# Kernel optimization log

Hardware: AMD Instinct MI355X
Metric: run time of the kernel (lower is better)

The kernel has to match this reference:

```python
import jax, jax.numpy as jnp
import numpy as np

INPUT_SIZE = 512
HIDDEN_SIZE = 512


def setup_inputs() -> dict:
    key = jax.random.key(0)
    k1, k2, k3, k4, k5 = jax.random.split(key, 5)
    B, N = 8, 2048
    x = jax.random.normal(k1, (B, N, INPUT_SIZE), dtype=jnp.float32)
    # Linear params (torch nn.Linear: y = x @ W^T + b), init scale ~ 1/sqrt(fan_in)
    s = 1.0 / np.sqrt(INPUT_SIZE)
    Wq = jax.random.uniform(k2, (HIDDEN_SIZE, INPUT_SIZE), minval=-s, maxval=s, dtype=jnp.float32)
    bq = jax.random.uniform(k3, (HIDDEN_SIZE,), minval=-s, maxval=s, dtype=jnp.float32)
    Wk = jax.random.uniform(k4, (HIDDEN_SIZE, INPUT_SIZE), minval=-s, maxval=s, dtype=jnp.float32)
    bk = jax.random.uniform(k5, (HIDDEN_SIZE,), minval=-s, maxval=s, dtype=jnp.float32)
    return {"x": x, "Wq": Wq, "bq": bq, "Wk": Wk, "bk": bk}


def reference(x, Wq, bq, Wk, bk):
    # q, k: [B, N, H]
    q = jnp.einsum('bnd,hd->bnh', x, Wq) + bq
    k = jnp.einsum('bnd,hd->bnh', x, Wk) + bk
    # scores: [B, N, N], softmax over last axis (dim=2)
    scores = jnp.einsum('bnh,bmh->bnm', q, k) / jnp.sqrt(jnp.float32(HIDDEN_SIZE))
    attn = jax.nn.softmax(scores, axis=2)
    # attended = attn^T @ x : [B, N, input_size]; squeeze(2) no-op since input_size>1
    attended = jnp.einsum('bnm,bnd->bmd', attn, x)
    return attended
```

## Files before the change

kernel.cpp:

```cpp
#include <hip/hip_runtime.h>

typedef __bf16 bf16x8 __attribute__((ext_vector_type(8)));
typedef float f32x4 __attribute__((ext_vector_type(4)));

__device__ __forceinline__ ushort f2bf(float f) {
    union { float f; unsigned u; } v; v.f = f;
    unsigned r = v.u + 0x7FFF + ((v.u >> 16) & 1);
    return (ushort)(r >> 16);
}

__device__ __forceinline__ void async_copy16(const void* g, void* l) {
    __builtin_amdgcn_global_load_lds(
        (const __attribute__((address_space(1))) void*)g,
        (__attribute__((address_space(3))) void*)l, 16, 0, 0);
}

__global__ __launch_bounds__(256) void cvt_kernel(
    const float4* __restrict__ x, const float4* __restrict__ Wq,
    const float4* __restrict__ Wk, const float4* __restrict__ bq,
    const float4* __restrict__ bk,
    ushort4* __restrict__ xb, ushort4* __restrict__ Wb,
    float4* __restrict__ biasc) {
    int i = blockIdx.x * 256 + threadIdx.x;
    if (i < 2097152) {
        float4 v = x[i];
        ushort4 r; r.x = f2bf(v.x); r.y = f2bf(v.y); r.z = f2bf(v.z); r.w = f2bf(v.w);
        xb[i] = r;
    }
    if (i < 131072) {
        float4 v = (i < 65536) ? Wq[i] : Wk[i - 65536];
        ushort4 r; r.x = f2bf(v.x); r.y = f2bf(v.y); r.z = f2bf(v.z); r.w = f2bf(v.w);
        Wb[i] = r;
    }
    if (i < 256) {
        biasc[i] = (i < 128) ? bq[i] : bk[i - 128];
    }
}

__global__ __launch_bounds__(256) void fold_kernel(
    const float* __restrict__ x, const float* __restrict__ Z,
    ushort* __restrict__ xzT) {
    __shared__ float tile[64][65];
    __shared__ float zin[64];
    const int b = blockIdx.y;
    const int td = blockIdx.x & 7;
    const int tn = blockIdx.x >> 3;
    const int n0 = tn * 64, d0 = td * 64;
    const int t = threadIdx.x;
    if (t < 64) zin[t] = 1.0f / Z[b * 2048 + n0 + t];
    __syncthreads();
    const int c = t & 63, r0 = t >> 6;
#pragma unroll
    for (int j = 0; j < 16; ++j) {
        int r = r0 + j * 4;
        tile[r][c] = x[((size_t)b * 2048 + n0 + r) * 512 + d0 + c] * zin[r];
    }
    __syncthreads();
#pragma unroll
    for (int j = 0; j < 16; ++j) {
        int dr = r0 + j * 4;
        xzT[((size_t)b * 512 + d0 + dr) * 2048 + n0 + c] = f2bf(tile[c][dr]);
    }
}

template <int EPI>
__global__ __launch_bounds__(256) void gemm_bt(
    const ushort* __restrict__ A, int lda, long sA,
    const ushort* __restrict__ B, int ldb, long sB,
    void* __restrict__ C, int ldc, long sC,
    int M, int N, int K,
    const float* __restrict__ bias, float scale,
    float* __restrict__ Z, long sZ) {
    __shared__ ushort lA[128 * 64];
    __shared__ ushort lB[128 * 64];
    const int b = blockIdx.y;
    A += (size_t)b * sA;
    B += (size_t)b * sB;
    const int tiles_n = N >> 7;
    const int tm = blockIdx.x / tiles_n, tn = blockIdx.x % tiles_n;
    const int t = threadIdx.x;
    const int l = t & 63, w = t >> 6;
    const int wr = w >> 1, wc = w & 1;

    f32x4 acc[4][4];
#pragma unroll
    for (int i = 0; i < 4; ++i)
#pragma unroll
        for (int j = 0; j < 4; ++j) acc[i][j] = (f32x4){0.f, 0.f, 0.f, 0.f};

    for (int k0 = 0; k0 < K; k0 += 64) {
#pragma unroll
        for (int p = 0; p < 4; ++p) {
            int off = p * 4096 + t * 16;
            int row = off >> 7;
            int kb = off & 127;
            int kswz = kb ^ ((row & 7) << 4);
            const ushort* srcA = A + (size_t)(tm * 128 + row) * lda + k0 + (kswz >> 1);
            async_copy16(srcA, (char*)lA + off);
            const ushort* srcB = B + (size_t)(tn * 128 + row) * ldb + k0 + (kswz >> 1);
            async_copy16(srcB, (char*)lB + off);
        }
        __syncthreads();
#pragma unroll
        for (int ks = 0; ks < 2; ++ks) {
            bf16x8 af[4], bfr[4];
#pragma unroll
            for (int i = 0; i < 4; ++i) {
                int row = wr * 64 + i * 16 + (l & 15);
                int colb = (ks * 64 + (l >> 4) * 16) ^ ((row & 7) << 4);
                af[i] = *(const bf16x8*)((const char*)lA + row * 128 + colb);
            }
#pragma unroll
            for (int j = 0; j < 4; ++j) {
                int row = wc * 64 + j * 16 + (l & 15);
                int colb = (ks * 64 + (l >> 4) * 16) ^ ((row & 7) << 4);
                bfr[j] = *(const bf16x8*)((const char*)lB + row * 128 + colb);
            }
#pragma unroll
            for (int i = 0; i < 4; ++i)
#pragma unroll
                for (int j = 0; j < 4; ++j)
                    acc[i][j] = __builtin_amdgcn_mfma_f32_16x16x32_bf16(
                        af[i], bfr[j], acc[i][j], 0, 0, 0);
        }
        __syncthreads();
    }

    const int m_base = tm * 128 + wr * 64;
    const int n_base = tn * 128 + wc * 64;

    if (EPI == 0) {
        ushort* Cp = (ushort*)C + (size_t)b * sC;
#pragma unroll
        for (int i = 0; i < 4; ++i)
#pragma unroll
            for (int j = 0; j < 4; ++j)
#pragma unroll
                for (int q = 0; q < 4; ++q) {
                    int row = m_base + i * 16 + (l >> 4) * 4 + q;
                    int col = n_base + j * 16 + (l & 15);
                    Cp[(size_t)row * ldc + col] = f2bf(acc[i][j][q] + bias[col]);
                }
    } else if (EPI == 1) {
        ushort* Cp = (ushort*)C + (size_t)b * sC;
        float colsum[4] = {0.f, 0.f, 0.f, 0.f};
#pragma unroll
        for (int i = 0; i < 4; ++i)
#pragma unroll
            for (int j = 0; j < 4; ++j)
#pragma unroll
                for (int q = 0; q < 4; ++q) {
                    int row = m_base + i * 16 + (l >> 4) * 4 + q;
                    int col = n_base + j * 16 + (l & 15);
                    float e = __expf(acc[i][j][q] * scale);
                    Cp[(size_t)row * ldc + col] = f2bf(e);
                    colsum[j] += e;
                }
#pragma unroll
        for (int j = 0; j < 4; ++j) {
            float s = colsum[j];
            s += __shfl_xor(s, 16);
            s += __shfl_xor(s, 32);
            if (l < 16) atomicAdd(&Z[b * sZ + n_base + j * 16 + l], s);
        }
    } else {
        float* Cp = (float*)C + (size_t)b * sC;
#pragma unroll
        for (int i = 0; i < 4; ++i)
#pragma unroll
            for (int j = 0; j < 4; ++j)
#pragma unroll
                for (int q = 0; q < 4; ++q) {
                    int row = m_base + i * 16 + (l >> 4) * 4 + q;
                    int col = n_base + j * 16 + (l & 15);
                    Cp[(size_t)row * ldc + col] = acc[i][j][q];
                }
    }
}

extern "C" void kernel_launch(void* const* d_in, const int* in_sizes, int n_in,
                              void* d_out, int out_size, void* d_ws, size_t ws_size,
                              hipStream_t stream) {
    const float* x  = (const float*)d_in[0];
    const float* Wq = (const float*)d_in[1];
    const float* bq = (const float*)d_in[2];
    const float* Wk = (const float*)d_in[3];
    const float* bk = (const float*)d_in[4];

    char* ws = (char*)d_ws;
    ushort* xb    = (ushort*)(ws);
    ushort* Wb    = (ushort*)(ws + 16777216);
    float*  biasc = (float*) (ws + 17825792);
    float*  Z     = (float*) (ws + 17829888);
    ushort* qkb   = (ushort*)(ws + 17895424);
    ushort* E     = (ushort*)(ws + 51449856);
    ushort* xzT   = xb;

    hipMemsetAsync(Z, 0, 16384 * 4, stream);

    cvt_kernel<<<8192, 256, 0, stream>>>(
        (const float4*)x, (const float4*)Wq, (const float4*)Wk,
        (const float4*)bq, (const float4*)bk,
        (ushort4*)xb, (ushort4*)Wb, (float4*)biasc);

    gemm_bt<0><<<dim3(1024, 1), 256, 0, stream>>>(
        xb, 512, 0L, Wb, 512, 0L, qkb, 1024, 0L,
        16384, 1024, 512, biasc, 0.f, nullptr, 0L);

    gemm_bt<1><<<dim3(256, 8), 256, 0, stream>>>(
        qkb + 512, 1024, 2048L * 1024, qkb, 1024, 2048L * 1024,
        E, 2048, 2048L * 2048, 2048, 2048, 512,
        nullptr, 0.04419417382415922f, Z, 2048L);

    fold_kernel<<<dim3(256, 8), 256, 0, stream>>>(x, Z, xzT);

    gemm_bt<2><<<dim3(64, 8), 256, 0, stream>>>(
        E, 2048, 2048L * 2048, xzT, 2048, 512L * 2048,
        d_out, 512, 2048L * 512, 2048, 512, 2048,
        nullptr, 0.f, nullptr, 0L);
}
```

Before: 154.4 us.

## Rewrite GEMMs as 8-wave 256-row tiles with double-buffered async LDS pipeline

Replaces the 128x128 single-buffered GEMM with an 8-wave (512-thread) kernel using 256xBN tiles, dynamic shared memory, and double-buffered global-to-LDS async copies. The copies are interleaved with MFMA phases through explicit waitcnt, barriers and setprio, so loads overlap compute. A new swizzle layout is used for the K-halves. Larger tiles increase data reuse per block but reduce block count (e.g. 256 blocks for the projection, 256 for the last GEMM), which risks poor CU occupancy on a 256-CU device and adds heavy register pressure.

```diff
diff --git a/kernel.cpp b/kernel.cpp
--- a/kernel.cpp
+++ b/kernel.cpp
@@ -63,119 +63,189 @@
     }
 }
 
-template <int EPI>
-__global__ __launch_bounds__(256) void gemm_bt(
+template <int BN, int EPI>
+__global__ __launch_bounds__(512, 2) void gemm8(
     const ushort* __restrict__ A, int lda, long sA,
     const ushort* __restrict__ B, int ldb, long sB,
     void* __restrict__ C, int ldc, long sC,
-    int M, int N, int K,
+    int tiles_n, int K,
     const float* __restrict__ bias, float scale,
     float* __restrict__ Z, long sZ) {
-    __shared__ ushort lA[128 * 64];
-    __shared__ ushort lB[128 * 64];
+    constexpr int NREP = BN / 64;
+    constexpr int JW = NREP / 2;
+    constexpr int LB = BN / 128;
+    constexpr int VMN = 4 + 2 * LB;
+    constexpr int ABUF = 32768;
+    constexpr int BHALF = BN * 64;
+    constexpr int BBUF = 2 * BHALF;
+    extern __shared__ char smem[];
+    char* lA = smem;
+    char* lB = smem + 2 * ABUF;
+
     const int b = blockIdx.y;
-    A += (size_t)b * sA;
-    B += (size_t)b * sB;
-    const int tiles_n = N >> 7;
+    const ushort* Ag = A + (size_t)b * sA;
+    const ushort* Bg = B + (size_t)b * sB;
     const int tm = blockIdx.x / tiles_n, tn = blockIdx.x % tiles_n;
     const int t = threadIdx.x;
     const int l = t & 63, w = t >> 6;
-    const int wr = w >> 1, wc = w & 1;
-
-    f32x4 acc[4][4];
-#pragma unroll
-    for (int i = 0; i < 4; ++i)
-#pragma unroll
-        for (int j = 0; j < 4; ++j) acc[i][j] = (f32x4){0.f, 0.f, 0.f, 0.f};
-
-    for (int k0 = 0; k0 < K; k0 += 64) {
-#pragma unroll
-        for (int p = 0; p < 4; ++p) {
-            int off = p * 4096 + t * 16;
-            int row = off >> 7;
-            int kb = off & 127;
-            int kswz = kb ^ ((row & 7) << 4);
-            const ushort* srcA = A + (size_t)(tm * 128 + row) * lda + k0 + (kswz >> 1);
-            async_copy16(srcA, (char*)lA + off);
-            const ushort* srcB = B + (size_t)(tn * 128 + row) * ldb + k0 + (kswz >> 1);
-            async_copy16(srcB, (char*)lB + off);
+    const int wr = w >> 2, wc = w & 3;
+    const int NT = K >> 6;
+
+    size_t gA[2]; int dA[2];
+#pragma unroll
+    for (int p = 0; p < 2; ++p) {
+        int off = p * 8192 + t * 16;
+        int row = off >> 6, kb = off & 63;
+        int kbs = kb ^ ((row & 6) << 3);
+        gA[p] = (size_t)(tm * 256 + row) * lda + (kbs >> 1);
+        dA[p] = off;
+    }
+    size_t gB[LB]; int dB[LB];
+#pragma unroll
+    for (int p = 0; p < LB; ++p) {
+        int off = p * 8192 + t * 16;
+        int row = off >> 6, kb = off & 63;
+        int kbs = kb ^ ((row & 6) << 3);
+        gB[p] = (size_t)(tn * BN + row) * ldb + (kbs >> 1);
+        dB[p] = off;
+    }
+
+    auto stageA = [&](int db, int ks, int ktt) {
+        if (ktt > NT - 1) ktt = NT - 1;
+        const ushort* s0 = Ag + ktt * 64 + ks * 32;
+#pragma unroll
+        for (int p = 0; p < 2; ++p)
+            async_copy16(s0 + gA[p], lA + db * ABUF + ks * 16384 + dA[p]);
+    };
+    auto stageB = [&](int db, int ks, int ktt) {
+        if (ktt > NT - 1) ktt = NT - 1;
+        const ushort* s0 = Bg + ktt * 64 + ks * 32;
+#pragma unroll
+        for (int p = 0; p < LB; ++p)
+            async_copy16(s0 + gB[p], lB + db * BBUF + ks * BHALF + dB[p]);
+    };
+
+    const int lan = (l & 15) * 64 + ((((l >> 4)) ^ ((l >> 1) & 3)) << 4);
+
+    f32x4 acc[8][NREP];
+#pragma unroll
+    for (int i = 0; i < 8; ++i)
+#pragma unroll
+        for (int j = 0; j < NREP; ++j) acc[i][j] = (f32x4){0.f, 0.f, 0.f, 0.f};
+
+    stageA(0, 0, 0); stageB(0, 0, 0);
+    stageA(0, 1, 0); stageB(0, 1, 0);
+    stageA(1, 0, 1); stageB(1, 0, 1);
+    asm volatile("s_waitcnt vmcnt(%0)" :: "n"(VMN) : "memory");
+    __builtin_amdgcn_s_barrier();
+    __builtin_amdgcn_sched_barrier(0);
+
+    for (int kt = 0; kt < NT; ++kt) {
+        const int db = kt & 1;
+        bf16x8 a[8];
+#pragma unroll
+        for (int ph = 0; ph < 4; ++ph) {
+            const int ks = ph >> 1;
+            const int js = (ph == 1 || ph == 2) ? 1 : 0;
+            if (ph == 0 || ph == 2) {
+#pragma unroll
+                for (int i = 0; i < 8; ++i)
+                    a[i] = *(const bf16x8*)(lA + db * ABUF + ks * 16384 +
+                                            wr * 8192 + i * 1024 + lan);
+            }
+            bf16x8 bb[JW];
+#pragma unroll
+            for (int j = 0; j < JW; ++j)
+                bb[j] = *(const bf16x8*)(lB + db * BBUF + ks * BHALF +
+                                         wc * (BN / 4) * 64 + (js * JW + j) * 1024 + lan);
+            if (ph == 0)      stageA(db ^ 1, 1, kt + 1);
+            else if (ph == 1) stageB(db ^ 1, 1, kt + 1);
+            else if (ph == 2) stageA(db, 0, kt + 2);
+            else              stageB(db, 0, kt + 2);
+            __builtin_amdgcn_sched_barrier(0);
+            if (ph == 1 || ph == 3)
+                asm volatile("s_waitcnt vmcnt(%0)" :: "n"(VMN) : "memory");
+            __builtin_amdgcn_s_barrier();
+            __builtin_amdgcn_s_setprio(1);
+#pragma unroll
+            for (int i = 0; i < 8; ++i)
+#pragma unroll
+                for (int j = 0; j < JW; ++j)
+                    acc[i][js * JW + j] = __builtin_amdgcn_mfma_f32_16x16x32_bf16(
+                        a[i], bb[j], acc[i][js * JW + j], 0, 0, 0);
+            __builtin_amdgcn_s_setprio(0);
+            __builtin_amdgcn_s_barrier();
+            __builtin_amdgcn_sched_barrier(0);
         }
-        __syncthreads();
-#pragma unroll
-        for (int ks = 0; ks < 2; ++ks) {
-            bf16x8 af[4], bfr[4];
-#pragma unroll
-            for (int i = 0; i < 4; ++i) {
-                int row = wr * 64 + i * 16 + (l & 15);
-                int colb = (ks * 64 + (l >> 4) * 16) ^ ((row & 7) << 4);
-                af[i] = *(const bf16x8*)((const char*)lA + row * 128 + colb);
-            }
-#pragma unroll
-            for (int j = 0; j < 4; ++j) {
-                int row = wc * 64 + j * 16 + (l & 15);
-                int colb = (ks * 64 + (l >> 4) * 16) ^ ((row & 7) << 4);
-                bfr[j] = *(const bf16x8*)((const char*)lB + row * 128 + colb);
-            }
-#pragma unroll
-            for (int i = 0; i < 4; ++i)
-#pragma unroll
-                for (int j = 0; j < 4; ++j)
-                    acc[i][j] = __builtin_amdgcn_mfma_f32_16x16x32_bf16(
-                        af[i], bfr[j], acc[i][j], 0, 0, 0);
-        }
-        __syncthreads();
-    }
-
-    const int m_base = tm * 128 + wr * 64;
-    const int n_base = tn * 128 + wc * 64;
+    }
+    asm volatile("s_waitcnt vmcnt(0)" ::: "memory");
+
+    const int mb = tm * 256 + wr * 128;
+    const int nb = tn * BN + wc * (BN / 4);
 
     if (EPI == 0) {
         ushort* Cp = (ushort*)C + (size_t)b * sC;
 #pragma unroll
-        for (int i = 0; i < 4; ++i)
-#pragma unroll
-            for (int j = 0; j < 4; ++j)
+        for (int i = 0; i < 8; ++i)
+#pragma unroll
+            for (int j = 0; j < NREP; ++j)
 #pragma unroll
                 for (int q = 0; q < 4; ++q) {
-                    int row = m_base + i * 16 + (l >> 4) * 4 + q;
-                    int col = n_base + j * 16 + (l & 15);
+                    int row = mb + i * 16 + (l >> 4) * 4 + q;
+                    int col = nb + j * 16 + (l & 15);
                     Cp[(size_t)row * ldc + col] = f2bf(acc[i][j][q] + bias[col]);
                 }
     } else if (EPI == 1) {
         ushort* Cp = (ushort*)C + (size_t)b * sC;
-        float colsum[4] = {0.f, 0.f, 0.f, 0.f};
-#pragma unroll
-        for (int i = 0; i < 4; ++i)
-#pragma unroll
-            for (int j = 0; j < 4; ++j)
+        float colsum[NREP];
+#pragma unroll
+        for (int j = 0; j < NREP; ++j) colsum[j] = 0.f;
+#pragma unroll
+        for (int i = 0; i < 8; ++i)
+#pragma unroll
+            for (int j = 0; j < NREP; ++j)
 #pragma unroll
                 for (int q = 0; q < 4; ++q) {
-                    int row = m_base + i * 16 + (l >> 4) * 4 + q;
-                    int col = n_base + j * 16 + (l & 15);
+                    int row = mb + i * 16 + (l >> 4) * 4 + q;
+                    int col = nb + j * 16 + (l & 15);
                     float e = __expf(acc[i][j][q] * scale);
                     Cp[(size_t)row * ldc + col] = f2bf(e);
                     colsum[j] += e;
                 }
 #pragma unroll
-        for (int j = 0; j < 4; ++j) {
+        for (int j = 0; j < NREP; ++j) {
             float s = colsum[j];
             s += __shfl_xor(s, 16);
             s += __shfl_xor(s, 32);
-            if (l < 16) atomicAdd(&Z[b * sZ + n_base + j * 16 + l], s);
+            if (l < 16) atomicAdd(&Z[b * sZ + nb + j * 16 + l], s);
         }
     } else {
         float* Cp = (float*)C + (size_t)b * sC;
 #pragma unroll
-        for (int i = 0; i < 4; ++i)
-#pragma unroll
-            for (int j = 0; j < 4; ++j)
+        for (int i = 0; i < 8; ++i)
+#pragma unroll
+            for (int j = 0; j < NREP; ++j)
 #pragma unroll
                 for (int q = 0; q < 4; ++q) {
-                    int row = m_base + i * 16 + (l >> 4) * 4 + q;
-                    int col = n_base + j * 16 + (l & 15);
+                    int row = mb + i * 16 + (l >> 4) * 4 + q;
+                    int col = nb + j * 16 + (l & 15);
                     Cp[(size_t)row * ldc + col] = acc[i][j][q];
                 }
     }
+}
+
+namespace {
+struct AttrInit {
+    AttrInit() {
+        hipFuncSetAttribute(reinterpret_cast<const void*>(&gemm8<256, 0>),
+                            hipFuncAttributeMaxDynamicSharedMemorySize, 131072);
+        hipFuncSetAttribute(reinterpret_cast<const void*>(&gemm8<256, 1>),
+                            hipFuncAttributeMaxDynamicSharedMemorySize, 131072);
+        hipFuncSetAttribute(reinterpret_cast<const void*>(&gemm8<128, 2>),
+                            hipFuncAttributeMaxDynamicSharedMemorySize, 98304);
+    }
+};
+AttrInit attr_init_;
 }
 
 extern "C" void kernel_launch(void* const* d_in, const int* in_sizes, int n_in,
@@ -203,19 +273,19 @@
         (const float4*)bq, (const float4*)bk,
         (ushort4*)xb, (ushort4*)Wb, (float4*)biasc);
 
-    gemm_bt<0><<<dim3(1024, 1), 256, 0, stream>>>(
+    gemm8<256, 0><<<dim3(256, 1), 512, 131072, stream>>>(
         xb, 512, 0L, Wb, 512, 0L, qkb, 1024, 0L,
-        16384, 1024, 512, biasc, 0.f, nullptr, 0L);
-
-    gemm_bt<1><<<dim3(256, 8), 256, 0, stream>>>(
+        4, 512, biasc, 0.f, nullptr, 0L);
+
+    gemm8<256, 1><<<dim3(64, 8), 512, 131072, stream>>>(
         qkb + 512, 1024, 2048L * 1024, qkb, 1024, 2048L * 1024,
-        E, 2048, 2048L * 2048, 2048, 2048, 512,
+        E, 2048, 2048L * 2048, 8, 512,
         nullptr, 0.04419417382415922f, Z, 2048L);
 
     fold_kernel<<<dim3(256, 8), 256, 0, stream>>>(x, Z, xzT);
 
-    gemm_bt<2><<<dim3(64, 8), 256, 0, stream>>>(
+    gemm8<128, 2><<<dim3(32, 8), 512, 98304, stream>>>(
         E, 2048, 2048L * 2048, xzT, 2048, 512L * 2048,
-        d_out, 512, 2048L * 512, 2048, 512, 2048,
+        d_out, 512, 2048L * 512, 4, 2048,
         nullptr, 0.f, nullptr, 0L);
 }
```

Result: no change. 156.4 us (+1.3%).

## Switch GEMMs to 32x32x16 MFMA and read bf16 x in fold kernel

Applied to the files above, without the earlier changes.

Replaces the 16x16x32 bf16 MFMA tiles with 32x32x16 MFMA in all three GEMMs, with a matching epilogue layout. This reduces LDS fragment loads per MFMA and the instruction count. The fold kernel now reads the bf16 copy of x with vectorized ushort4 loads and stores, instead of fp32 x with scalar stores, which cuts its memory traffic. Its output is written into the qkb buffer, since xb is now read. Using bf16 x in the fold adds a second rounding step.

```diff
diff --git a/kernel.cpp b/kernel.cpp
--- a/kernel.cpp
+++ b/kernel.cpp
@@ -1,12 +1,16 @@
 #include <hip/hip_runtime.h>
 
 typedef __bf16 bf16x8 __attribute__((ext_vector_type(8)));
-typedef float f32x4 __attribute__((ext_vector_type(4)));
+typedef float f32x16 __attribute__((ext_vector_type(16)));
 
 __device__ __forceinline__ ushort f2bf(float f) {
     union { float f; unsigned u; } v; v.f = f;
     unsigned r = v.u + 0x7FFF + ((v.u >> 16) & 1);
     return (ushort)(r >> 16);
+}
+__device__ __forceinline__ float bf2f(ushort u) {
+    union { unsigned u; float f; } v; v.u = ((unsigned)u) << 16;
+    return v.f;
 }
 
 __device__ __forceinline__ void async_copy16(const void* g, void* l) {
@@ -38,7 +42,7 @@
 }
 
 __global__ __launch_bounds__(256) void fold_kernel(
-    const float* __restrict__ x, const float* __restrict__ Z,
+    const ushort* __restrict__ xb, const float* __restrict__ Z,
     ushort* __restrict__ xzT) {
     __shared__ float tile[64][65];
     __shared__ float zin[64];
@@ -49,26 +53,36 @@
     const int t = threadIdx.x;
     if (t < 64) zin[t] = 1.0f / Z[b * 2048 + n0 + t];
     __syncthreads();
-    const int c = t & 63, r0 = t >> 6;
-#pragma unroll
-    for (int j = 0; j < 16; ++j) {
-        int r = r0 + j * 4;
-        tile[r][c] = x[((size_t)b * 2048 + n0 + r) * 512 + d0 + c] * zin[r];
+    const int c4 = (t & 15) * 4, rr = t >> 4;
+#pragma unroll
+    for (int j = 0; j < 4; ++j) {
+        int nr = rr + j * 16;
+        ushort4 v = *(const ushort4*)&xb[((size_t)b * 2048 + n0 + nr) * 512 + d0 + c4];
+        float zi = zin[nr];
+        tile[nr][c4 + 0] = bf2f(v.x) * zi;
+        tile[nr][c4 + 1] = bf2f(v.y) * zi;
+        tile[nr][c4 + 2] = bf2f(v.z) * zi;
+        tile[nr][c4 + 3] = bf2f(v.w) * zi;
     }
     __syncthreads();
 #pragma unroll
-    for (int j = 0; j < 16; ++j) {
-        int dr = r0 + j * 4;
-        xzT[((size_t)b * 512 + d0 + dr) * 2048 + n0 + c] = f2bf(tile[c][dr]);
+    for (int j = 0; j < 4; ++j) {
+        int dr = rr + j * 16;
+        ushort4 r;
+        r.x = f2bf(tile[c4 + 0][dr]);
+        r.y = f2bf(tile[c4 + 1][dr]);
+        r.z = f2bf(tile[c4 + 2][dr]);
+        r.w = f2bf(tile[c4 + 3][dr]);
+        *(ushort4*)&xzT[((size_t)b * 512 + d0 + dr) * 2048 + n0 + c4] = r;
     }
 }
 
 template <int EPI>
-__global__ __launch_bounds__(256) void gemm_bt(
+__global__ __launch_bounds__(256) void gemm_bt32(
     const ushort* __restrict__ A, int lda, long sA,
     const ushort* __restrict__ B, int ldb, long sB,
     void* __restrict__ C, int ldc, long sC,
-    int M, int N, int K,
+    int tiles_n, int K,
     const float* __restrict__ bias, float scale,
     float* __restrict__ Z, long sZ) {
     __shared__ ushort lA[128 * 64];
@@ -76,105 +90,114 @@
     const int b = blockIdx.y;
     A += (size_t)b * sA;
     B += (size_t)b * sB;
-    const int tiles_n = N >> 7;
     const int tm = blockIdx.x / tiles_n, tn = blockIdx.x % tiles_n;
     const int t = threadIdx.x;
     const int l = t & 63, w = t >> 6;
     const int wr = w >> 1, wc = w & 1;
 
-    f32x4 acc[4][4];
-#pragma unroll
-    for (int i = 0; i < 4; ++i)
-#pragma unroll
-        for (int j = 0; j < 4; ++j) acc[i][j] = (f32x4){0.f, 0.f, 0.f, 0.f};
+    f32x16 acc[2][2];
+#pragma unroll
+    for (int i = 0; i < 2; ++i)
+#pragma unroll
+        for (int j = 0; j < 2; ++j)
+#pragma unroll
+            for (int q = 0; q < 16; ++q) acc[i][j][q] = 0.f;
+
+    const int soff = t * 16;
+    const int srow0 = soff >> 7;
+    const int skb = soff & 127;
 
     for (int k0 = 0; k0 < K; k0 += 64) {
 #pragma unroll
         for (int p = 0; p < 4; ++p) {
-            int off = p * 4096 + t * 16;
-            int row = off >> 7;
-            int kb = off & 127;
-            int kswz = kb ^ ((row & 7) << 4);
-            const ushort* srcA = A + (size_t)(tm * 128 + row) * lda + k0 + (kswz >> 1);
-            async_copy16(srcA, (char*)lA + off);
-            const ushort* srcB = B + (size_t)(tn * 128 + row) * ldb + k0 + (kswz >> 1);
-            async_copy16(srcB, (char*)lB + off);
+            int off = p * 4096 + soff;
+            int row = srow0 + p * 32;
+            int kswz = skb ^ ((row & 7) << 4);
+            async_copy16(A + (size_t)(tm * 128 + row) * lda + k0 + (kswz >> 1),
+                         (char*)lA + off);
+            async_copy16(B + (size_t)(tn * 128 + row) * ldb + k0 + (kswz >> 1),
+                         (char*)lB + off);
         }
         __syncthreads();
 #pragma unroll
-        for (int ks = 0; ks < 2; ++ks) {
-            bf16x8 af[4], bfr[4];
-#pragma unroll
-            for (int i = 0; i < 4; ++i) {
-                int row = wr * 64 + i * 16 + (l & 15);
-                int colb = (ks * 64 + (l >> 4) * 16) ^ ((row & 7) << 4);
-                af[i] = *(const bf16x8*)((const char*)lA + row * 128 + colb);
-            }
-#pragma unroll
-            for (int j = 0; j < 4; ++j) {
-                int row = wc * 64 + j * 16 + (l & 15);
-                int colb = (ks * 64 + (l >> 4) * 16) ^ ((row & 7) << 4);
-                bfr[j] = *(const bf16x8*)((const char*)lB + row * 128 + colb);
-            }
-#pragma unroll
-            for (int i = 0; i < 4; ++i)
-#pragma unroll
-                for (int j = 0; j < 4; ++j)
-                    acc[i][j] = __builtin_amdgcn_mfma_f32_16x16x32_bf16(
-                        af[i], bfr[j], acc[i][j], 0, 0, 0);
+        for (int ksx = 0; ksx < 4; ++ksx) {
+            bf16x8 af[2], bfr[2];
+#pragma unroll
+            for (int rb = 0; rb < 2; ++rb) {
+                int row = wr * 64 + rb * 32 + (l & 31);
+                int colb = (ksx * 32 + (l >> 5) * 16) ^ ((row & 7) << 4);
+                af[rb] = *(const bf16x8*)((const char*)lA + row * 128 + colb);
+            }
+#pragma unroll
+            for (int cb = 0; cb < 2; ++cb) {
+                int row = wc * 64 + cb * 32 + (l & 31);
+                int colb = (ksx * 32 + (l >> 5) * 16) ^ ((row & 7) << 4);
+                bfr[cb] = *(const bf16x8*)((const char*)lB + row * 128 + colb);
+            }
+#pragma unroll
+            for (int rb = 0; rb < 2; ++rb)
+#pragma unroll
+                for (int cb = 0; cb < 2; ++cb)
+                    acc[rb][cb] = __builtin_amdgcn_mfma_f32_32x32x16_bf16(
+                        af[rb], bfr[cb], acc[rb][cb], 0, 0, 0);
         }
         __syncthreads();
     }
 
-    const int m_base = tm * 128 + wr * 64;
-    const int n_base = tn * 128 + wc * 64;
+    const int mb = tm * 128 + wr * 64;
+    const int nb = tn * 128 + wc * 64;
+    const int rbase = 4 * (l >> 5);
+    const int cl = l & 31;
 
     if (EPI == 0) {
         ushort* Cp = (ushort*)C + (size_t)b * sC;
 #pragma unroll
-        for (int i = 0; i < 4; ++i)
-#pragma unroll
-            for (int j = 0; j < 4; ++j)
-#pragma unroll
-                for (int q = 0; q < 4; ++q) {
-                    int row = m_base + i * 16 + (l >> 4) * 4 + q;
-                    int col = n_base + j * 16 + (l & 15);
-                    Cp[(size_t)row * ldc + col] = f2bf(acc[i][j][q] + bias[col]);
+        for (int rb = 0; rb < 2; ++rb)
+#pragma unroll
+            for (int cb = 0; cb < 2; ++cb) {
+                int col = nb + cb * 32 + cl;
+                float bv = bias[col];
+#pragma unroll
+                for (int reg = 0; reg < 16; ++reg) {
+                    int row = mb + rb * 32 + (reg & 3) + 8 * (reg >> 2) + rbase;
+                    Cp[(size_t)row * ldc + col] = f2bf(acc[rb][cb][reg] + bv);
                 }
+            }
     } else if (EPI == 1) {
         ushort* Cp = (ushort*)C + (size_t)b * sC;
-        float colsum[4] = {0.f, 0.f, 0.f, 0.f};
-#pragma unroll
-        for (int i = 0; i < 4; ++i)
-#pragma unroll
-            for (int j = 0; j < 4; ++j)
-#pragma unroll
-                for (int q = 0; q < 4; ++q) {
-                    int row = m_base + i * 16 + (l >> 4) * 4 + q;
-                    int col = n_base + j * 16 + (l & 15);
-                    float e = __expf(acc[i][j][q] * scale);
+        float cs[2] = {0.f, 0.f};
+#pragma unroll
+        for (int rb = 0; rb < 2; ++rb)
+#pragma unroll
+            for (int cb = 0; cb < 2; ++cb) {
+                int col = nb + cb * 32 + cl;
+#pragma unroll
+                for (int reg = 0; reg < 16; ++reg) {
+                    int row = mb + rb * 32 + (reg & 3) + 8 * (reg >> 2) + rbase;
+                    float e = __expf(acc[rb][cb][reg] * scale);
                     Cp[(size_t)row * ldc + col] = f2bf(e);
-                    colsum[j] += e;
+                    cs[cb] += e;
                 }
-#pragma unroll
-        for (int j = 0; j < 4; ++j) {
-            float s = colsum[j];
-            s += __shfl_xor(s, 16);
+            }
+#pragma unroll
+        for (int cb = 0; cb < 2; ++cb) {
+            float s = cs[cb];
             s += __shfl_xor(s, 32);
-            if (l < 16) atomicAdd(&Z[b * sZ + n_base + j * 16 + l], s);
+            if (l < 32) atomicAdd(&Z[b * sZ + nb + cb * 32 + cl], s);
         }
     } else {
         float* Cp = (float*)C + (size_t)b * sC;
 #pragma unroll
-        for (int i = 0; i < 4; ++i)
-#pragma unroll
-            for (int j = 0; j < 4; ++j)
-#pragma unroll
-                for (int q = 0; q < 4; ++q) {
-                    int row = m_base + i * 16 + (l >> 4) * 4 + q;
-                    int col = n_base + j * 16 + (l & 15);
-                    Cp[(size_t)row * ldc + col] = acc[i][j][q];
+        for (int rb = 0; rb < 2; ++rb)
+#pragma unroll
+            for (int cb = 0; cb < 2; ++cb) {
+                int col = nb + cb * 32 + cl;
+#pragma unroll
+                for (int reg = 0; reg < 16; ++reg) {
+                    int row = mb + rb * 32 + (reg & 3) + 8 * (reg >> 2) + rbase;
+                    Cp[(size_t)row * ldc + col] = acc[rb][cb][reg];
                 }
+            }
     }
 }
 
@@ -194,7 +217,7 @@
     float*  Z     = (float*) (ws + 17829888);
     ushort* qkb   = (ushort*)(ws + 17895424);
     ushort* E     = (ushort*)(ws + 51449856);
-    ushort* xzT   = xb;
+    ushort* xzT   = qkb;
 
     hipMemsetAsync(Z, 0, 16384 * 4, stream);
 
@@ -203,19 +226,19 @@
         (const float4*)bq, (const float4*)bk,
         (ushort4*)xb, (ushort4*)Wb, (float4*)biasc);
 
-    gemm_bt<0><<<dim3(1024, 1), 256, 0, stream>>>(
+    gemm_bt32<0><<<dim3(1024, 1), 256, 0, stream>>>(
         xb, 512, 0L, Wb, 512, 0L, qkb, 1024, 0L,
-        16384, 1024, 512, biasc, 0.f, nullptr, 0L);
-
-    gemm_bt<1><<<dim3(256, 8), 256, 0, stream>>>(
+        8, 512, biasc, 0.f, nullptr, 0L);
+
+    gemm_bt32<1><<<dim3(256, 8), 256, 0, stream>>>(
         qkb + 512, 1024, 2048L * 1024, qkb, 1024, 2048L * 1024,
-        E, 2048, 2048L * 2048, 2048, 2048, 512,
+        E, 2048, 2048L * 2048, 16, 512,
         nullptr, 0.04419417382415922f, Z, 2048L);
 
-    fold_kernel<<<dim3(256, 8), 256, 0, stream>>>(x, Z, xzT);
-
-    gemm_bt<2><<<dim3(64, 8), 256, 0, stream>>>(
+    fold_kernel<<<dim3(256, 8), 256, 0, stream>>>(xb, Z, xzT);
+
+    gemm_bt32<2><<<dim3(64, 8), 256, 0, stream>>>(
         E, 2048, 2048L * 2048, xzT, 2048, 512L * 2048,
-        d_out, 512, 2048L * 512, 2048, 512, 2048,
+        d_out, 512, 2048L * 512, 4, 2048,
         nullptr, 0.f, nullptr, 0L);
 }
```

New measurement: 153.8 us. About the same (-0.3%).

## Double-buffer GEMM LDS tiles and read bf16 x in fold kernel

Applied to the files above, without the earlier changes.

The GEMM kernel now keeps two LDS buffers and issues the async global-to-LDS copies for the next K tile before computing on the current one, so loads can overlap MFMA work. Global offsets are precomputed once, and one sync per iteration is kept. The fold kernel now reads the already converted bf16 x with vectorized loads and writes ushort4, instead of reading fp32 x one element at a time, which halves its input traffic. Its output goes into the qkb region so the bf16 x buffer stays intact. LDS use doubles, which may lower occupancy. Scaling the bf16-rounded x by 1/Z then rounding again adds one more rounding step.

```diff
diff --git a/kernel.cpp b/kernel.cpp
--- a/kernel.cpp
+++ b/kernel.cpp
@@ -7,6 +7,10 @@
     union { float f; unsigned u; } v; v.f = f;
     unsigned r = v.u + 0x7FFF + ((v.u >> 16) & 1);
     return (ushort)(r >> 16);
+}
+__device__ __forceinline__ float bf2f(ushort u) {
+    union { unsigned u; float f; } v; v.u = ((unsigned)u) << 16;
+    return v.f;
 }
 
 __device__ __forceinline__ void async_copy16(const void* g, void* l) {
@@ -38,7 +42,7 @@
 }
 
 __global__ __launch_bounds__(256) void fold_kernel(
-    const float* __restrict__ x, const float* __restrict__ Z,
+    const ushort* __restrict__ xb, const float* __restrict__ Z,
     ushort* __restrict__ xzT) {
     __shared__ float tile[64][65];
     __shared__ float zin[64];
@@ -49,58 +53,83 @@
     const int t = threadIdx.x;
     if (t < 64) zin[t] = 1.0f / Z[b * 2048 + n0 + t];
     __syncthreads();
-    const int c = t & 63, r0 = t >> 6;
-#pragma unroll
-    for (int j = 0; j < 16; ++j) {
-        int r = r0 + j * 4;
-        tile[r][c] = x[((size_t)b * 2048 + n0 + r) * 512 + d0 + c] * zin[r];
+    const int c4 = (t & 15) * 4, rr = t >> 4;
+#pragma unroll
+    for (int j = 0; j < 4; ++j) {
+        int nr = rr + j * 16;
+        ushort4 v = *(const ushort4*)&xb[((size_t)b * 2048 + n0 + nr) * 512 + d0 + c4];
+        float zi = zin[nr];
+        tile[nr][c4 + 0] = bf2f(v.x) * zi;
+        tile[nr][c4 + 1] = bf2f(v.y) * zi;
+        tile[nr][c4 + 2] = bf2f(v.z) * zi;
+        tile[nr][c4 + 3] = bf2f(v.w) * zi;
     }
     __syncthreads();
 #pragma unroll
-    for (int j = 0; j < 16; ++j) {
-        int dr = r0 + j * 4;
-        xzT[((size_t)b * 512 + d0 + dr) * 2048 + n0 + c] = f2bf(tile[c][dr]);
+    for (int j = 0; j < 4; ++j) {
+        int dr = rr + j * 16;
+        ushort4 r;
+        r.x = f2bf(tile[c4 + 0][dr]);
+        r.y = f2bf(tile[c4 + 1][dr]);
+        r.z = f2bf(tile[c4 + 2][dr]);
+        r.w = f2bf(tile[c4 + 3][dr]);
+        *(ushort4*)&xzT[((size_t)b * 512 + d0 + dr) * 2048 + n0 + c4] = r;
     }
 }
 
 template <int EPI>
-__global__ __launch_bounds__(256) void gemm_bt(
+__global__ __launch_bounds__(256) void gemm_db(
     const ushort* __restrict__ A, int lda, long sA,
     const ushort* __restrict__ B, int ldb, long sB,
     void* __restrict__ C, int ldc, long sC,
-    int M, int N, int K,
+    int tiles_n, int K,
     const float* __restrict__ bias, float scale,
     float* __restrict__ Z, long sZ) {
-    __shared__ ushort lA[128 * 64];
-    __shared__ ushort lB[128 * 64];
+    __shared__ ushort lA[2][8192];
+    __shared__ ushort lB[2][8192];
     const int b = blockIdx.y;
     A += (size_t)b * sA;
     B += (size_t)b * sB;
-    const int tiles_n = N >> 7;
     const int tm = blockIdx.x / tiles_n, tn = blockIdx.x % tiles_n;
     const int t = threadIdx.x;
     const int l = t & 63, w = t >> 6;
     const int wr = w >> 1, wc = w & 1;
 
+    size_t gA[4], gB[4];
+    int dOf[4];
+#pragma unroll
+    for (int p = 0; p < 4; ++p) {
+        int off = p * 4096 + t * 16;
+        int row = off >> 7;
+        int kb = off & 127;
+        int kswz = kb ^ ((row & 7) << 4);
+        gA[p] = (size_t)(tm * 128 + row) * lda + (kswz >> 1);
+        gB[p] = (size_t)(tn * 128 + row) * ldb + (kswz >> 1);
+        dOf[p] = off;
+    }
+
+    auto stage = [&](int buf, int k0) {
+#pragma unroll
+        for (int p = 0; p < 4; ++p) {
+            async_copy16(A + gA[p] + k0, (char*)lA[buf] + dOf[p]);
+            async_copy16(B + gB[p] + k0, (char*)lB[buf] + dOf[p]);
+        }
+    };
+
     f32x4 acc[4][4];
 #pragma unroll
     for (int i = 0; i < 4; ++i)
 #pragma unroll
         for (int j = 0; j < 4; ++j) acc[i][j] = (f32x4){0.f, 0.f, 0.f, 0.f};
 
-    for (int k0 = 0; k0 < K; k0 += 64) {
-#pragma unroll
-        for (int p = 0; p < 4; ++p) {
-            int off = p * 4096 + t * 16;
-            int row = off >> 7;
-            int kb = off & 127;
-            int kswz = kb ^ ((row & 7) << 4);
-            const ushort* srcA = A + (size_t)(tm * 128 + row) * lda + k0 + (kswz >> 1);
-            async_copy16(srcA, (char*)lA + off);
-            const ushort* srcB = B + (size_t)(tn * 128 + row) * ldb + k0 + (kswz >> 1);
-            async_copy16(srcB, (char*)lB + off);
-        }
-        __syncthreads();
+    stage(0, 0);
+    __syncthreads();
+
+    const int nk = K >> 6;
+    for (int kt = 0; kt < nk; ++kt) {
+        const int cur = kt & 1;
+        if (kt + 1 < nk) stage(cur ^ 1, (kt + 1) << 6);
+        __builtin_amdgcn_sched_barrier(0);
 #pragma unroll
         for (int ks = 0; ks < 2; ++ks) {
             bf16x8 af[4], bfr[4];
@@ -108,13 +137,13 @@
             for (int i = 0; i < 4; ++i) {
                 int row = wr * 64 + i * 16 + (l & 15);
                 int colb = (ks * 64 + (l >> 4) * 16) ^ ((row & 7) << 4);
-                af[i] = *(const bf16x8*)((const char*)lA + row * 128 + colb);
+                af[i] = *(const bf16x8*)((const char*)lA[cur] + row * 128 + colb);
             }
 #pragma unroll
             for (int j = 0; j < 4; ++j) {
                 int row = wc * 64 + j * 16 + (l & 15);
                 int colb = (ks * 64 + (l >> 4) * 16) ^ ((row & 7) << 4);
-                bfr[j] = *(const bf16x8*)((const char*)lB + row * 128 + colb);
+                bfr[j] = *(const bf16x8*)((const char*)lB[cur] + row * 128 + colb);
             }
 #pragma unroll
             for (int i = 0; i < 4; ++i)
@@ -126,8 +155,8 @@
         __syncthreads();
     }
 
-    const int m_base = tm * 128 + wr * 64;
-    const int n_base = tn * 128 + wc * 64;
+    const int mb = tm * 128 + wr * 64;
+    const int nb = tn * 128 + wc * 64;
 
     if (EPI == 0) {
         ushort* Cp = (ushort*)C + (size_t)b * sC;
@@ -137,8 +166,8 @@
             for (int j = 0; j < 4; ++j)
 #pragma unroll
                 for (int q = 0; q < 4; ++q) {
-                    int row = m_base + i * 16 + (l >> 4) * 4 + q;
-                    int col = n_base + j * 16 + (l & 15);
+                    int row = mb + i * 16 + (l >> 4) * 4 + q;
+                    int col = nb + j * 16 + (l & 15);
                     Cp[(size_t)row * ldc + col] = f2bf(acc[i][j][q] + bias[col]);
                 }
     } else if (EPI == 1) {
@@ -150,8 +179,8 @@
             for (int j = 0; j < 4; ++j)
 #pragma unroll
                 for (int q = 0; q < 4; ++q) {
-                    int row = m_base + i * 16 + (l >> 4) * 4 + q;
-                    int col = n_base + j * 16 + (l & 15);
+                    int row = mb + i * 16 + (l >> 4) * 4 + q;
+                    int col = nb + j * 16 + (l & 15);
                     float e = __expf(acc[i][j][q] * scale);
                     Cp[(size_t)row * ldc + col] = f2bf(e);
                     colsum[j] += e;
@@ -161,7 +190,7 @@
             float s = colsum[j];
             s += __shfl_xor(s, 16);
             s += __shfl_xor(s, 32);
-            if (l < 16) atomicAdd(&Z[b * sZ + n_base + j * 16 + l], s);
+            if (l < 16) atomicAdd(&Z[b * sZ + nb + j * 16 + l], s);
         }
     } else {
         float* Cp = (float*)C + (size_t)b * sC;
@@ -171,8 +200,8 @@
             for (int j = 0; j < 4; ++j)
 #pragma unroll
                 for (int q = 0; q < 4; ++q) {
-                    int row = m_base + i * 16 + (l >> 4) * 4 + q;
-                    int col = n_base + j * 16 + (l & 15);
+                    int row = mb + i * 16 + (l >> 4) * 4 + q;
+                    int col = nb + j * 16 + (l & 15);
                     Cp[(size_t)row * ldc + col] = acc[i][j][q];
                 }
     }
@@ -194,7 +223,7 @@
     float*  Z     = (float*) (ws + 17829888);
     ushort* qkb   = (ushort*)(ws + 17895424);
     ushort* E     = (ushort*)(ws + 51449856);
-    ushort* xzT   = xb;
+    ushort* xzT   = qkb;
 
     hipMemsetAsync(Z, 0, 16384 * 4, stream);
 
@@ -203,19 +232,19 @@
         (const float4*)bq, (const float4*)bk,
         (ushort4*)xb, (ushort4*)Wb, (float4*)biasc);
 
-    gemm_bt<0><<<dim3(1024, 1), 256, 0, stream>>>(
+    gemm_db<0><<<dim3(1024, 1), 256, 0, stream>>>(
         xb, 512, 0L, Wb, 512, 0L, qkb, 1024, 0L,
-        16384, 1024, 512, biasc, 0.f, nullptr, 0L);
-
-    gemm_bt<1><<<dim3(256, 8), 256, 0, stream>>>(
+        8, 512, biasc, 0.f, nullptr, 0L);
+
+    gemm_db<1><<<dim3(256, 8), 256, 0, stream>>>(
         qkb + 512, 1024, 2048L * 1024, qkb, 1024, 2048L * 1024,
-        E, 2048, 2048L * 2048, 2048, 2048, 512,
+        E, 2048, 2048L * 2048, 16, 512,
         nullptr, 0.04419417382415922f, Z, 2048L);
 
-    fold_kernel<<<dim3(256, 8), 256, 0, stream>>>(x, Z, xzT);
-
-    gemm_bt<2><<<dim3(64, 8), 256, 0, stream>>>(
+    fold_kernel<<<dim3(256, 8), 256, 0, stream>>>(xb, Z, xzT);
+
+    gemm_db<2><<<dim3(64, 8), 256, 0, stream>>>(
         E, 2048, 2048L * 2048, xzT, 2048, 512L * 2048,
-        d_out, 512, 2048L * 512, 2048, 512, 2048,
+        d_out, 512, 2048L * 512, 4, 2048,
         nullptr, 0.f, nullptr, 0L);
 }
```

Result: no change. 153.7 us (-0.4%).
